# Kernel tuning notes

Measured on AMD Instinct MI355X. Metric: run time of the kernel, lower is better.

The kernel has to match this reference:

```python
import jax, jax.numpy as jnp
import numpy as np

BINS = 30
MMT = 0.75
LOSS_WEIGHT = 1.0
N, C = 2000000, 16


def setup_inputs() -> dict:
    key = jax.random.key(0)
    k1, k2 = jax.random.split(key)
    pred = jax.random.normal(k1, (N, C), dtype=jnp.float32)
    target = jax.random.randint(k2, (N, C), 0, 2, dtype=jnp.int32)
    acc_sum = jnp.zeros((BINS,), dtype=jnp.float32)
    return {"pred": pred, "target": target, "acc_sum": acc_sum}


def reference(pred, target, acc_sum):
    t = target.astype(pred.dtype)
    tot = float(pred.size)

    # gradient density g = |sigmoid(pred) - target|, detached
    g = jnp.abs(jax.nn.sigmoid(jax.lax.stop_gradient(pred)) - t)

    # edges are i/BINS, last edge bumped by 1e-6 => bin = floor(g*BINS), clipped
    idx = jnp.clip((g * BINS).astype(jnp.int32), 0, BINS - 1)  # [N, C]

    flat_idx = idx.reshape(-1)
    counts = jax.ops.segment_sum(
        jnp.ones_like(flat_idx, dtype=pred.dtype), flat_idx, num_segments=BINS
    )  # [BINS]

    nonempty = counts > 0
    new_acc = jnp.where(nonempty, MMT * acc_sum + (1.0 - MMT) * counts, acc_sum)
    safe_acc = jnp.where(nonempty, new_acc, jnp.ones_like(new_acc))

    n = jnp.maximum(jnp.sum(nonempty).astype(pred.dtype), 1.0)
    per_bin_w = tot / safe_acc / n  # [BINS]
    weights = jax.lax.stop_gradient(per_bin_w[idx])  # [N, C]

    # stable BCE with logits: t*softplus(-x) + (1-t)*softplus(x)
    bce = t * jax.nn.softplus(-pred) + (1.0 - t) * jax.nn.softplus(pred)
    loss = jnp.sum(bce * weights) / tot
    return loss * LOSS_WEIGHT
```

## Files before the change

kernel.cpp:

```cpp
#include <hip/hip_runtime.h>

#define BINS 30
#define MMT 0.75f
#define LOSS_WEIGHT 1.0f

#define RSTRIDE 31
#define NTHREADS 256
#define NROWS (NTHREADS / 2)
#define HWORDS (NROWS * RSTRIDE)
#define CNT_ONE (1u << 20)
#define SUM_MASK 0xFFFFFu
#define SSCALE 256.0f
#define INV_SSCALE (1.0f / 256.0f)


__device__ __forceinline__ void ghm_elem(float x, int tt, unsigned int* __restrict__ row) {
    float z = tt ? -x : x;
    float a = __expf(-fabsf(z));
    float h = 1.0f + a;
    float r = __builtin_amdgcn_rcpf(h);
    float g = (z >= 0.0f) ? r : 1.0f - r;
    float sp = fmaxf(z, 0.0f) + __logf(h);
    int b = (int)(g * 30.0f);
    b = b > (BINS - 1) ? (BINS - 1) : b;
    b = b < 0 ? 0 : b;
    atomicAdd(&row[b], (unsigned int)(sp * SSCALE + 0.5f) + CNT_ONE);
}

__global__ __launch_bounds__(NTHREADS, 4) void ghmc_pass1(
                           const float4* __restrict__ pred4,
                           const int4*   __restrict__ tgt4,
                           float*        __restrict__ gS,
                           unsigned int* __restrict__ gC,
                           unsigned int* __restrict__ gDone,
                           const float*  __restrict__ acc_sum,
                           float*        __restrict__ out,
                           int ngrp, int total, float tot) {
    __shared__ unsigned int sH[HWORDS];
    __shared__ unsigned int sPs[4 * BINS];
    __shared__ unsigned int sPc[4 * BINS];
    __shared__ unsigned int sLast;
    const int t = threadIdx.x;

    for (int k = t; k < HWORDS; k += NTHREADS) sH[k] = 0u;
    __syncthreads();

    unsigned int* const row = &sH[(t >> 1) * RSTRIDE];

    const int gs = gridDim.x * blockDim.x;
    int g = blockIdx.x * blockDim.x + t;
    if (g < ngrp) {
        float4 p0 = pred4[2 * g],     p1 = pred4[2 * g + 1];
        int4   q0 = tgt4[2 * g],      q1 = tgt4[2 * g + 1];
        for (;;) {
            int  gn   = g + gs;
            bool more = (gn < ngrp);
            int  gl   = more ? gn : g;
            float4 p0n = pred4[2 * gl],  p1n = pred4[2 * gl + 1];
            int4   q0n = tgt4[2 * gl],   q1n = tgt4[2 * gl + 1];
            #pragma unroll
            for (int j = 0; j < 4; ++j) ghm_elem((&p0.x)[j], (&q0.x)[j], row);
            #pragma unroll
            for (int j = 0; j < 4; ++j) ghm_elem((&p1.x)[j], (&q1.x)[j], row);
            if (!more) break;
            p0 = p0n; p1 = p1n; q0 = q0n; q1 = q1n; g = gn;
        }
    }

    if (blockIdx.x == 0 && t == 0) {
        const float* predf = (const float*)pred4;
        const int*   tgtf  = (const int*)tgt4;
        for (int e = ngrp * 8; e < total; ++e) ghm_elem(predf[e], tgtf[e], row);
    }
    __syncthreads();

    {
        const int w = t >> 6;
        const int l = t & 63;
        if (l < BINS) {
            unsigned int cs = 0u, ss = 0u;
            const int r0 = w * (NROWS / 4);
            #pragma unroll 8
            for (int r2 = 0; r2 < NROWS / 4; ++r2) {
                unsigned int v = sH[(r0 + r2) * RSTRIDE + l];
                cs += v >> 20;
                ss += v & SUM_MASK;
            }
            sPs[w * BINS + l] = ss;
            sPc[w * BINS + l] = cs;
        }
    }
    __syncthreads();

    if (t < BINS) {
        unsigned int cs = 0u, ss = 0u;
        #pragma unroll
        for (int w = 0; w < 4; ++w) {
            ss += sPs[w * BINS + t];
            cs += sPc[w * BINS + t];
        }
        if (cs != 0u) {
            atomicAdd(&gS[t], (float)ss * INV_SSCALE);
            atomicAdd(&gC[t], cs);
        }
        __threadfence();
    }
    __syncthreads();

    if (t == 0) sLast = (atomicAdd(gDone, 1u) == (unsigned int)(gridDim.x - 1)) ? 1u : 0u;
    __syncthreads();
    if (sLast && t < 64) {
        unsigned int c = 0u; float s = 0.0f;
        if (t < BINS) {
            c = atomicAdd(&gC[t], 0u);
            s = atomicAdd(&gS[t], 0.0f);
        }
        unsigned long long m = __ballot(t < BINS && c != 0u);
        float nf = fmaxf((float)__popcll(m), 1.0f);
        float term = 0.0f;
        if (t < BINS && c != 0u) {
            float na = MMT * acc_sum[t] + (1.0f - MMT) * (float)c;
            term = (tot / na / nf) * s;
        }
        float loss = 0.0f;
        for (int b = 0; b < BINS; ++b) loss += __shfl(term, b);
        if (t == 0) out[0] = (loss / tot) * LOSS_WEIGHT;
    }
}

extern "C" void kernel_launch(void* const* d_in, const int* in_sizes, int n_in,
                              void* d_out, int out_size, void* d_ws, size_t ws_size,
                              hipStream_t stream) {
    const float* pred    = (const float*)d_in[0];
    const int*   target  = (const int*)d_in[1];
    const float* acc_sum = (const float*)d_in[2];

    const int total = in_sizes[0];
    const int ngrp  = total / 8;

    float*        gS    = (float*)d_ws;
    unsigned int* gC    = (unsigned int*)((char*)d_ws + 256);
    unsigned int* gDone = (unsigned int*)((char*)d_ws + 512);

    hipMemsetAsync(d_ws, 0, 768, stream);

    const int blocks = 1024;
    ghmc_pass1<<<blocks, NTHREADS, 0, stream>>>(
        (const float4*)pred, (const int4*)target, gS, gC, gDone, acc_sum,
        (float*)d_out, ngrp, total, (float)total);
}
```

Measured before the change: 311.6 us.

## Replace shared-memory atomic histogram with per-thread cumulative threshold counters

Instead of computing the sigmoid and doing an LDS atomicAdd into a binned histogram per element, each thread keeps 30 register accumulators. It adds the packed (count, loss) value to every bin whose logit threshold the signed input exceeds, which builds a cumulative histogram with no atomics. The last block recovers per-bin values by differencing adjacent cumulative bins through a lane shuffle. This trades LDS atomic contention for about 30 compare-and-add VALU ops per element and more registers, and it also drops the explicit software prefetch in the main loop.

Result: no change. 314.5 us (+1.0%).

```diff
diff --git a/kernel.cpp b/kernel.cpp
--- a/kernel.cpp
+++ b/kernel.cpp
@@ -6,25 +6,31 @@
 
 #define RSTRIDE 31
 #define NTHREADS 256
-#define NROWS (NTHREADS / 2)
-#define HWORDS (NROWS * RSTRIDE)
+#define HWORDS (NTHREADS * RSTRIDE)
 #define CNT_ONE (1u << 20)
 #define SUM_MASK 0xFFFFFu
 #define SSCALE 256.0f
 #define INV_SSCALE (1.0f / 256.0f)
 
 
-__device__ __forceinline__ void ghm_elem(float x, int tt, unsigned int* __restrict__ row) {
-    float z = tt ? -x : x;
-    float a = __expf(-fabsf(z));
-    float h = 1.0f + a;
-    float r = __builtin_amdgcn_rcpf(h);
-    float g = (z >= 0.0f) ? r : 1.0f - r;
+__device__ __forceinline__ void ghm_elem(float x, int tt, unsigned int (&acc)[BINS]) {
+    constexpr float TK[BINS] = {
+        0.0f,
+        -3.3672958f, -2.6390573f, -2.1972246f, -1.8718022f, -1.6094379f,
+        -1.3862944f, -1.1895841f, -1.0116009f, -0.84729786f, -0.69314718f,
+        -0.54654371f, -0.40546511f, -0.26826399f, -0.13353139f, 0.0f,
+         0.13353139f, 0.26826399f, 0.40546511f, 0.54654371f, 0.69314718f,
+         0.84729786f, 1.0116009f, 1.1895841f, 1.3862944f, 1.6094379f,
+         1.8718022f, 2.1972246f, 2.6390573f, 3.3672958f };
+    float z  = __uint_as_float(__float_as_uint(x) ^ ((unsigned int)tt << 31));
+    float e  = __expf(-fabsf(z));
+    float h  = 1.0f + e;
     float sp = fmaxf(z, 0.0f) + __logf(h);
-    int b = (int)(g * 30.0f);
-    b = b > (BINS - 1) ? (BINS - 1) : b;
-    b = b < 0 ? 0 : b;
-    atomicAdd(&row[b], (unsigned int)(sp * SSCALE + 0.5f) + CNT_ONE);
+    unsigned int v = (unsigned int)(sp * SSCALE + 0.5f) + CNT_ONE;
+    acc[0] += v;
+    #pragma unroll
+    for (int k = 1; k < BINS; ++k)
+        acc[k] += (z >= TK[k]) ? v : 0u;
 }
 
 __global__ __launch_bounds__(NTHREADS, 4) void ghmc_pass1(
@@ -35,42 +41,37 @@
                            unsigned int* __restrict__ gDone,
                            const float*  __restrict__ acc_sum,
                            float*        __restrict__ out,
-                           int ngrp, int total, float tot) {
+                           int nvec, int total, float tot) {
     __shared__ unsigned int sH[HWORDS];
     __shared__ unsigned int sPs[4 * BINS];
     __shared__ unsigned int sPc[4 * BINS];
     __shared__ unsigned int sLast;
     const int t = threadIdx.x;
 
-    for (int k = t; k < HWORDS; k += NTHREADS) sH[k] = 0u;
-    __syncthreads();
+    unsigned int acc[BINS];
+    #pragma unroll
+    for (int k = 0; k < BINS; ++k) acc[k] = 0u;
 
-    unsigned int* const row = &sH[(t >> 1) * RSTRIDE];
-
-    const int gs = gridDim.x * blockDim.x;
-    int g = blockIdx.x * blockDim.x + t;
-    if (g < ngrp) {
-        float4 p0 = pred4[2 * g],     p1 = pred4[2 * g + 1];
-        int4   q0 = tgt4[2 * g],      q1 = tgt4[2 * g + 1];
-        for (;;) {
-            int  gn   = g + gs;
-            bool more = (gn < ngrp);
-            int  gl   = more ? gn : g;
-            float4 p0n = pred4[2 * gl],  p1n = pred4[2 * gl + 1];
-            int4   q0n = tgt4[2 * gl],   q1n = tgt4[2 * gl + 1];
-            #pragma unroll
-            for (int j = 0; j < 4; ++j) ghm_elem((&p0.x)[j], (&q0.x)[j], row);
-            #pragma unroll
-            for (int j = 0; j < 4; ++j) ghm_elem((&p1.x)[j], (&q1.x)[j], row);
-            if (!more) break;
-            p0 = p0n; p1 = p1n; q0 = q0n; q1 = q1n; g = gn;
-        }
+    const int stride = gridDim.x * blockDim.x;
+    for (int i = blockIdx.x * blockDim.x + t; i < nvec; i += stride) {
+        float4 p  = pred4[i];
+        int4   tv = tgt4[i];
+        ghm_elem(p.x, tv.x, acc);
+        ghm_elem(p.y, tv.y, acc);
+        ghm_elem(p.z, tv.z, acc);
+        ghm_elem(p.w, tv.w, acc);
     }
 
     if (blockIdx.x == 0 && t == 0) {
         const float* predf = (const float*)pred4;
         const int*   tgtf  = (const int*)tgt4;
-        for (int e = ngrp * 8; e < total; ++e) ghm_elem(predf[e], tgtf[e], row);
+        for (int e = nvec * 4; e < total; ++e) ghm_elem(predf[e], tgtf[e], acc);
+    }
+
+    {
+        unsigned int* rowp = &sH[t * RSTRIDE];
+        #pragma unroll
+        for (int k = 0; k < BINS; ++k) rowp[k] = acc[k];
     }
     __syncthreads();
 
@@ -79,9 +80,9 @@
         const int l = t & 63;
         if (l < BINS) {
             unsigned int cs = 0u, ss = 0u;
-            const int r0 = w * (NROWS / 4);
+            const int r0 = w * 64;
             #pragma unroll 8
-            for (int r2 = 0; r2 < NROWS / 4; ++r2) {
+            for (int r2 = 0; r2 < 64; ++r2) {
                 unsigned int v = sH[(r0 + r2) * RSTRIDE + l];
                 cs += v >> 20;
                 ss += v & SUM_MASK;
@@ -110,10 +111,17 @@
     if (t == 0) sLast = (atomicAdd(gDone, 1u) == (unsigned int)(gridDim.x - 1)) ? 1u : 0u;
     __syncthreads();
     if (sLast && t < 64) {
-        unsigned int c = 0u; float s = 0.0f;
+        unsigned int f = 0u; float gsum = 0.0f;
         if (t < BINS) {
-            c = atomicAdd(&gC[t], 0u);
-            s = atomicAdd(&gS[t], 0.0f);
+            f    = atomicAdd(&gC[t], 0u);
+            gsum = atomicAdd(&gS[t], 0.0f);
+        }
+        unsigned int fn = __shfl(f, (t + 1) & 63);
+        float        gn = __shfl(gsum, (t + 1) & 63);
+        unsigned int c  = 0u; float s = 0.0f;
+        if (t < BINS) {
+            c = (t == BINS - 1) ? f : f - fn;
+            s = (t == BINS - 1) ? gsum : gsum - gn;
         }
         unsigned long long m = __ballot(t < BINS && c != 0u);
         float nf = fmaxf((float)__popcll(m), 1.0f);
@@ -136,7 +144,7 @@
     const float* acc_sum = (const float*)d_in[2];
 
     const int total = in_sizes[0];
-    const int ngrp  = total / 8;
+    const int nvec  = total / 4;
 
     float*        gS    = (float*)d_ws;
     unsigned int* gC    = (unsigned int*)((char*)d_ws + 256);
@@ -147,5 +155,5 @@
     const int blocks = 1024;
     ghmc_pass1<<<blocks, NTHREADS, 0, stream>>>(
         (const float4*)pred, (const int4*)target, gS, gC, gDone, acc_sum,
-        (float*)d_out, ngrp, total, (float)total);
+        (float*)d_out, nvec, total, (float)total);
 }
```

## Deepen load pipeline with inline-asm 4-stage prefetch and manual vmcnt waits

Applied to the files above, without the earlier changes.

Each thread's single-ahead prefetch of 8-element groups is replaced by a 4-slot rotating pipeline of 16-byte pred/target loads. The loads are issued through inline global_load_dwordx4 and consumed after s_waitcnt vmcnt(6), which keeps three groups in flight per thread. This is meant to hide HBM latency in a memory-bound histogram pass. It also swaps the target-conditional negate for a sign-bit XOR. The cost is more registers and hand-written waitcnt logic that the compiler cannot check, plus redundant clamped loads for out-of-range iterations.

Measured after the change: 316.6 us. No clear change (+1.6%).

```diff
diff --git a/kernel.cpp b/kernel.cpp
--- a/kernel.cpp
+++ b/kernel.cpp
@@ -13,9 +13,24 @@
 #define SSCALE 256.0f
 #define INV_SSCALE (1.0f / 256.0f)
 
+typedef __attribute__((ext_vector_type(4))) float f32x4;
+typedef __attribute__((ext_vector_type(4))) int   i32x4;
+
+
+__device__ __forceinline__ void issue2(unsigned long long pa, unsigned long long ta,
+                                       f32x4& P, i32x4& Q) {
+    asm volatile(
+        "global_load_dwordx4 %0, %2, off\n\t"
+        "global_load_dwordx4 %1, %3, off"
+        : "=&v"(P), "=&v"(Q)
+        : "v"(pa), "v"(ta)
+        : "memory");
+}
+#define WAITV6() do { asm volatile("s_waitcnt vmcnt(6)" ::: "memory"); \
+                      __builtin_amdgcn_sched_barrier(0); } while (0)
 
 __device__ __forceinline__ void ghm_elem(float x, int tt, unsigned int* __restrict__ row) {
-    float z = tt ? -x : x;
+    float z = __uint_as_float(__float_as_uint(x) ^ ((unsigned int)tt << 31));
     float a = __expf(-fabsf(z));
     float h = 1.0f + a;
     float r = __builtin_amdgcn_rcpf(h);
@@ -35,7 +50,7 @@
                            unsigned int* __restrict__ gDone,
                            const float*  __restrict__ acc_sum,
                            float*        __restrict__ out,
-                           int ngrp, int total, float tot) {
+                           int ngrp, int nit, int total, float tot) {
     __shared__ unsigned int sH[HWORDS];
     __shared__ unsigned int sPs[4 * BINS];
     __shared__ unsigned int sPc[4 * BINS];
@@ -47,30 +62,50 @@
 
     unsigned int* const row = &sH[(t >> 1) * RSTRIDE];
 
-    const int gs = gridDim.x * blockDim.x;
-    int g = blockIdx.x * blockDim.x + t;
-    if (g < ngrp) {
-        float4 p0 = pred4[2 * g],     p1 = pred4[2 * g + 1];
-        int4   q0 = tgt4[2 * g],      q1 = tgt4[2 * g + 1];
-        for (;;) {
-            int  gn   = g + gs;
-            bool more = (gn < ngrp);
-            int  gl   = more ? gn : g;
-            float4 p0n = pred4[2 * gl],  p1n = pred4[2 * gl + 1];
-            int4   q0n = tgt4[2 * gl],   q1n = tgt4[2 * gl + 1];
-            #pragma unroll
-            for (int j = 0; j < 4; ++j) ghm_elem((&p0.x)[j], (&q0.x)[j], row);
-            #pragma unroll
-            for (int j = 0; j < 4; ++j) ghm_elem((&p1.x)[j], (&q1.x)[j], row);
-            if (!more) break;
-            p0 = p0n; p1 = p1n; q0 = q0n; q1 = q1n; g = gn;
-        }
+    const int stride = gridDim.x * blockDim.x;
+    const int g0 = blockIdx.x * blockDim.x + t;
+    const int gsafe = (g0 < ngrp) ? g0 : 0;
+    const unsigned long long pb = (unsigned long long)pred4;
+    const unsigned long long tb = (unsigned long long)tgt4;
+
+    #define GOFF(gg) ((unsigned long long)(((gg) < ngrp) ? (gg) : gsafe) * 16ull)
+
+    f32x4 P0, P1, P2, P3;
+    i32x4 Q0, Q1, Q2, Q3;
+
+    issue2(pb + GOFF(g0 + 0 * stride), tb + GOFF(g0 + 0 * stride), P0, Q0);
+    issue2(pb + GOFF(g0 + 1 * stride), tb + GOFF(g0 + 1 * stride), P1, Q1);
+    issue2(pb + GOFF(g0 + 2 * stride), tb + GOFF(g0 + 2 * stride), P2, Q2);
+
+    #define SLOT(PF_P, PF_Q, PF_K, CP_P, CP_Q, CP_K)                              \
+        do {                                                                      \
+            int gp = g0 + (it + (PF_K)) * stride;                                 \
+            issue2(pb + GOFF(gp), tb + GOFF(gp), PF_P, PF_Q);                     \
+            WAITV6();                                                             \
+            int gc = g0 + (it + (CP_K)) * stride;                                 \
+            if (gc < ngrp) {                                                      \
+                ghm_elem(CP_P[0], CP_Q[0], row);                                  \
+                ghm_elem(CP_P[1], CP_Q[1], row);                                  \
+                ghm_elem(CP_P[2], CP_Q[2], row);                                  \
+                ghm_elem(CP_P[3], CP_Q[3], row);                                  \
+            }                                                                     \
+        } while (0)
+
+    for (int it = 0; it < nit; it += 4) {
+        SLOT(P3, Q3, 3, P0, Q0, 0);
+        SLOT(P0, Q0, 4, P1, Q1, 1);
+        SLOT(P1, Q1, 5, P2, Q2, 2);
+        SLOT(P2, Q2, 6, P3, Q3, 3);
     }
+    #undef SLOT
+    #undef GOFF
+    asm volatile("s_waitcnt vmcnt(0)" ::: "memory");
+    __builtin_amdgcn_sched_barrier(0);
 
     if (blockIdx.x == 0 && t == 0) {
         const float* predf = (const float*)pred4;
         const int*   tgtf  = (const int*)tgt4;
-        for (int e = ngrp * 8; e < total; ++e) ghm_elem(predf[e], tgtf[e], row);
+        for (int e = ngrp * 4; e < total; ++e) ghm_elem(predf[e], tgtf[e], row);
     }
     __syncthreads();
 
@@ -136,7 +171,7 @@
     const float* acc_sum = (const float*)d_in[2];
 
     const int total = in_sizes[0];
-    const int ngrp  = total / 8;
+    const int ngrp  = total / 4;
 
     float*        gS    = (float*)d_ws;
     unsigned int* gC    = (unsigned int*)((char*)d_ws + 256);
@@ -145,7 +180,11 @@
     hipMemsetAsync(d_ws, 0, 768, stream);
 
     const int blocks = 1024;
+    const int stride = blocks * NTHREADS;
+    int nit = (ngrp + stride - 1) / stride;
+    nit = (nit + 3) & ~3;
+
     ghmc_pass1<<<blocks, NTHREADS, 0, stream>>>(
         (const float4*)pred, (const int4*)target, gS, gC, gDone, acc_sum,
-        (float*)d_out, ngrp, total, (float)total);
+        (float*)d_out, ngrp, nit, total, (float)total);
 }
```
